# Optimization experiments

Hardware: AMD Instinct MI355X
Metric: run time of the kernel (lower is better)

Reference implementation:

```python
import jax, jax.numpy as jnp
import numpy as np

NUM_AUDIOS = 64
NODES_PER = 800
N = NUM_AUDIOS * NODES_PER  # 51200
DEG = 8
E = N * DEG  # 409600
IN_C, HID, OUT, HEADS = 512, 256, 256, 2
NEG_SLOPE = 0.2  # PyG GATConv default


def setup_inputs() -> dict:
    key = jax.random.key(0)
    ks = jax.random.split(key, 12)
    x = jax.random.normal(ks[0], (N, IN_C), jnp.float32)
    # edges strictly inside each audio's node block (PyG batching: no cross-graph edges)
    src_l = jax.random.randint(ks[1], (NUM_AUDIOS, NODES_PER * DEG), 0, NODES_PER)
    dst_l = jax.random.randint(ks[2], (NUM_AUDIOS, NODES_PER * DEG), 0, NODES_PER)
    off = (jnp.arange(NUM_AUDIOS) * NODES_PER)[:, None]
    edge_index = jnp.stack([(src_l + off).reshape(-1), (dst_l + off).reshape(-1)]).astype(jnp.int32)
    batch = jnp.repeat(jnp.arange(NUM_AUDIOS), NODES_PER).astype(jnp.int32)

    def gl(k, shape, fan):
        return (jax.random.normal(k, shape, jnp.float32) / np.sqrt(fan)).astype(jnp.float32)

    W1 = gl(ks[3], (IN_C, HEADS * HID), IN_C)
    a_s1 = gl(ks[4], (HEADS, HID), HID)
    a_d1 = gl(ks[5], (HEADS, HID), HID)
    b1 = jnp.zeros((HID,), jnp.float32)
    W2 = gl(ks[6], (HID, HEADS * OUT), HID)
    a_s2 = gl(ks[7], (HEADS, OUT), OUT)
    a_d2 = gl(ks[8], (HEADS, OUT), OUT)
    b2 = jnp.zeros((OUT,), jnp.float32)
    w_att = gl(ks[9], (OUT, 1), OUT)
    b_att = jnp.zeros((1,), jnp.float32)
    w_cls = gl(ks[10], (OUT, 2), OUT)
    b_cls = jnp.zeros((2,), jnp.float32)
    return dict(x=x, edge_index=edge_index, batch=batch,
                W1=W1, a_s1=a_s1, a_d1=a_d1, b1=b1,
                W2=W2, a_s2=a_s2, a_d2=a_d2, b2=b2,
                w_att=w_att, b_att=b_att, w_cls=w_cls, b_cls=b_cls)


def _gat(x, src, dst, W, a_s, a_d, b):
    """PyG GATConv(heads=H, concat=False): linear -> per-edge LeakyReLU scores ->
    softmax over incoming edges (with self-loops) -> scatter-sum -> head-mean + bias."""
    n = x.shape[0]
    H, C = a_s.shape
    h = (x @ W).reshape(n, H, C)                      # [N,H,C]
    al_s = jnp.einsum('nhc,hc->nh', h, a_s)           # [N,H]
    al_d = jnp.einsum('nhc,hc->nh', h, a_d)
    loop = jnp.arange(n, dtype=src.dtype)             # add self-loops (default)
    s = jnp.concatenate([src, loop])
    d = jnp.concatenate([dst, loop])
    e = jax.nn.leaky_relu(al_s[s] + al_d[d], NEG_SLOPE)  # [E+N,H]
    mx = jax.ops.segment_max(e, d, num_segments=n)
    w = jnp.exp(e - mx[d])
    den = jax.ops.segment_sum(w, d, num_segments=n)
    alpha = w / den[d]
    out = jax.ops.segment_sum(h[s] * alpha[:, :, None], d, num_segments=n)  # [N,H,C]
    return out.mean(axis=1) + b


def reference(x, edge_index, batch, W1, a_s1, a_d1, b1, W2, a_s2, a_d2, b2,
              w_att, b_att, w_cls, b_cls):
    src, dst = edge_index[0], edge_index[1]
    h = jax.nn.relu(_gat(x, src, dst, W1, a_s1, a_d1, b1))
    node_emb = _gat(h, src, dst, W2, a_s2, a_d2, b2)
    # per-audio temporal attention: softmax over nodes within each audio segment.
    # (edges never cross audio boundaries, so the per-subgraph GAT re-run in the
    #  original Python loop equals the full-graph GAT restricted to each segment.)
    logits = node_emb @ w_att + b_att                 # [N,1]
    mx = jax.ops.segment_max(logits, batch, num_segments=NUM_AUDIOS)
    w = jnp.exp(logits - mx[batch])
    den = jax.ops.segment_sum(w, batch, num_segments=NUM_AUDIOS)
    attn = w / den[batch]                             # [N,1]
    attended = jax.ops.segment_sum(attn * node_emb, batch, num_segments=NUM_AUDIOS)  # [A,OUT]
    audio_result = attended @ w_cls + b_cls           # [A,2]
    return node_emb, audio_result
```

## Files before the change

kernel.cpp:

```cpp
#include <hip/hip_runtime.h>
#include <cstdint>
#include <cstddef>

#define NUM_AUDIOS 64
#define NODES_PER  800
#define NN         51200
#define EE         409600

typedef __attribute__((ext_vector_type(8))) unsigned short ushort8;
typedef __attribute__((ext_vector_type(4))) unsigned short ushort4v;
typedef __attribute__((ext_vector_type(8))) __bf16 bf16x8;
typedef __attribute__((ext_vector_type(4))) float f32x4;

__device__ __forceinline__ float b2f(unsigned short h) {
  return __uint_as_float(((unsigned)h) << 16);
}
__device__ __forceinline__ unsigned short f2b(float f) {
  unsigned u = __float_as_uint(f);
  u += 0x7fffu + ((u >> 16) & 1u);
  return (unsigned short)(u >> 16);
}
__device__ __forceinline__ float lrelu(float v) { return v > 0.f ? v : 0.2f * v; }

#define P_AS1 0
#define P_AD1 512
#define P_B1  1024
#define P_AS2 1536
#define P_AD2 2048
#define P_B2  2560
#define P_WATT 3072
#define P_BATT 3328
#define P_WCLS 3336
#define P_BCLS 3848

#define ZERO_F4 132096
#define ZERO_BLOCKS 516

__global__ __launch_bounds__(256) void prolog0_k(float4* __restrict__ zbase,
                                                 const unsigned short* __restrict__ x,
                                                 int* __restrict__ flag) {
  const int i = blockIdx.x * 256 + threadIdx.x;
  if (i < ZERO_F4) zbase[i] = (float4){0.f, 0.f, 0.f, 0.f};
  if (blockIdx.x == 0) {
    __shared__ int s;
    if (threadIdx.x == 0) s = 0;
    __syncthreads();
    int big = 0;
    for (int k = threadIdx.x; k < 4096; k += 256) {
      const float v = b2f(x[k]);
      if (!(__builtin_fabsf(v) <= 1e4f)) big = 1;
    }
    if (big) atomicOr(&s, 1);
    __syncthreads();
    if (threadIdx.x == 0) *flag = s;
  }
}

#define PB_CONV 25600
#define PB_PAR  (PB_CONV + 10)
#define PB_T1   (PB_PAR + 1024)
#define PB_T2   (PB_T1 + 512)
#define PB_HIST (PB_T2 + 1600)

__global__ __launch_bounds__(256) void prep_k(
    const void* __restrict__ xraw, unsigned short* __restrict__ x16,
    const void* __restrict__ W1, unsigned short* __restrict__ W1T,
    const void* __restrict__ W2, unsigned short* __restrict__ W2T,
    const void* p0, const void* p1, const void* p2, const void* p3, const void* p4,
    const void* p5, const void* p6, const void* p7, const void* p8, const void* p9,
    unsigned short* __restrict__ params,
    const int* __restrict__ dst, int* __restrict__ counts,
    const int* __restrict__ flagp) {
  const int b = blockIdx.x, tid = threadIdx.x;
  const int f = *flagp;
  if (b < PB_CONV) {
    const size_t i = ((size_t)b * 256 + tid) * 4;
    if (f) {
      const float4 v = *(const float4*)((const float*)xraw + i);
      ushort4v o;
      o[0] = f2b(v.x); o[1] = f2b(v.y); o[2] = f2b(v.z); o[3] = f2b(v.w);
      *(ushort4v*)(x16 + i) = o;
    } else {
      *(ushort4v*)(x16 + i) = *(const ushort4v*)((const unsigned short*)xraw + i);
    }
  } else if (b < PB_PAR) {
    const void* srcs[10] = {p0, p1, p2, p3, p4, p5, p6, p7, p8, p9};
    const int offs[10] = {P_AS1, P_AD1, P_B1, P_AS2, P_AD2, P_B2, P_WATT, P_BATT, P_WCLS, P_BCLS};
    const int lens[10] = {512, 512, 256, 512, 512, 256, 256, 1, 512, 2};
    const int s = b - PB_CONV;
    for (int i = tid; i < lens[s]; i += 256)
      params[offs[s] + i] = f ? f2b(((const float*)srcs[s])[i])
                              : ((const unsigned short*)srcs[s])[i];
  } else if (b < PB_T1) {
    const int idx = (b - PB_PAR) * 256 + tid;
    const int n = idx >> 9, k = idx & 511;
    W1T[idx] = f ? f2b(((const float*)W1)[(size_t)k * 512 + n])
                 : ((const unsigned short*)W1)[(size_t)k * 512 + n];
  } else if (b < PB_T2) {
    const int idx = (b - PB_T1) * 256 + tid;
    const int n = idx >> 8, k = idx & 255;
    W2T[idx] = f ? f2b(((const float*)W2)[(size_t)k * 512 + n])
                 : ((const unsigned short*)W2)[(size_t)k * 512 + n];
  } else {
    const int e = (b - PB_T2) * 256 + tid;
    atomicAdd(&counts[dst[e]], 1);
  }
}

__global__ __launch_bounds__(256) void rowptr_k(const int* __restrict__ counts, int* __restrict__ row_ptr) {
  __shared__ int sh[800];
  __shared__ int pre[200];
  const int a = blockIdx.x, t = threadIdx.x;
  for (int i = t; i < 800; i += 256) sh[i] = counts[a * 800 + i];
  __syncthreads();
  if (t < 200) pre[t] = sh[t * 4] + sh[t * 4 + 1] + sh[t * 4 + 2] + sh[t * 4 + 3];
  __syncthreads();
  if (t == 0) {
    int run = 0;
    for (int i = 0; i < 200; ++i) { const int v = pre[i]; pre[i] = run; run += v; }
  }
  __syncthreads();
  if (t < 200) {
    int b = a * 6400 + pre[t];
#pragma unroll
    for (int j = 0; j < 4; ++j) { row_ptr[a * 800 + t * 4 + j] = b; b += sh[t * 4 + j]; }
  }
}

__global__ __launch_bounds__(256) void scatter_k(const int* __restrict__ src, const int* __restrict__ dst,
                                                 const int* __restrict__ row_ptr, int* __restrict__ cursor,
                                                 int* __restrict__ ssrc) {
  const int e = blockIdx.x * 256 + threadIdx.x;
  const int d = dst[e];
  const int p = atomicAdd(&cursor[d], 1);
  ssrc[row_ptr[d] + p] = src[e];
}

__global__ __launch_bounds__(256) void gemm_bt(const unsigned short* __restrict__ A,
                                               const unsigned short* __restrict__ BT,
                                               unsigned short* __restrict__ C,
                                               int K, int Nn,
                                               const unsigned short* __restrict__ a_s,
                                               const unsigned short* __restrict__ a_d,
                                               float* __restrict__ al_s,
                                               float* __restrict__ al_d) {
  __shared__ unsigned short As[128 * 32];
  __shared__ unsigned short Bs[128 * 32];
  const int tid = threadIdx.x;
  const int wave = tid >> 6, lane = tid & 63;
  const int m0 = blockIdx.y * 128, n0 = blockIdx.x * 128;
  const int wm = wave >> 1, wn = wave & 1;
  const int row = lane & 15, quad = lane >> 4;
  f32x4 acc[4][4];
#pragma unroll
  for (int i = 0; i < 4; ++i)
#pragma unroll
    for (int j = 0; j < 4; ++j) acc[i][j] = (f32x4){0.f, 0.f, 0.f, 0.f};

  for (int k0 = 0; k0 < K; k0 += 32) {
#pragma unroll
    for (int r = 0; r < 2; ++r) {
      const int cc = r * 256 + wave * 64 + lane;
      const int arow = cc >> 2, kc = (cc & 3) * 8;
      __builtin_amdgcn_global_load_lds(
          (const __attribute__((address_space(1))) void*)(A + (size_t)(m0 + arow) * K + k0 + kc),
          (__attribute__((address_space(3))) void*)(As + (size_t)(r * 256 + wave * 64) * 8),
          16, 0, 0);
      __builtin_amdgcn_global_load_lds(
          (const __attribute__((address_space(1))) void*)(BT + (size_t)(n0 + arow) * K + k0 + kc),
          (__attribute__((address_space(3))) void*)(Bs + (size_t)(r * 256 + wave * 64) * 8),
          16, 0, 0);
    }
    __syncthreads();

    bf16x8 af[4], bq[4];
#pragma unroll
    for (int i = 0; i < 4; ++i) {
      af[i] = *(const bf16x8*)&As[(wm * 64 + i * 16 + row) * 32 + quad * 8];
      bq[i] = *(const bf16x8*)&Bs[(wn * 64 + i * 16 + row) * 32 + quad * 8];
    }
#pragma unroll
    for (int i = 0; i < 4; ++i)
#pragma unroll
      for (int j = 0; j < 4; ++j)
        acc[i][j] = __builtin_amdgcn_mfma_f32_16x16x32_bf16(af[i], bq[j], acc[i][j], 0, 0, 0);
    __syncthreads();
  }

  const int col = lane & 15;
#pragma unroll
  for (int i = 0; i < 4; ++i)
#pragma unroll
    for (int j = 0; j < 4; ++j)
#pragma unroll
      for (int r = 0; r < 4; ++r) {
        const int gm = m0 + wm * 64 + i * 16 + quad * 4 + r;
        const int gn = n0 + wn * 64 + j * 16 + col;
        C[(size_t)gm * Nn + gn] = f2b(acc[i][j][r]);
      }

  {
    const int head = (n0 + wn * 64) >> 8;
    float as4[4], ad4[4];
#pragma unroll
    for (int j = 0; j < 4; ++j) {
      const int gn = n0 + wn * 64 + j * 16 + col;
      as4[j] = b2f(a_s[gn]);
      ad4[j] = b2f(a_d[gn]);
    }
#pragma unroll
    for (int i = 0; i < 4; ++i)
#pragma unroll
      for (int r = 0; r < 4; ++r) {
        float ps = 0.f, pd = 0.f;
#pragma unroll
        for (int j = 0; j < 4; ++j) { ps += acc[i][j][r] * as4[j]; pd += acc[i][j][r] * ad4[j]; }
#pragma unroll
        for (int off = 1; off < 16; off <<= 1) {
          ps += __shfl_xor(ps, off);
          pd += __shfl_xor(pd, off);
        }
        if (col == 0) {
          const int gm = m0 + wm * 64 + i * 16 + quad * 4 + r;
          atomicAdd(&al_s[gm * 2 + head], ps);
          atomicAdd(&al_d[gm * 2 + head], pd);
        }
      }
  }
}

__global__ __launch_bounds__(256) void agg_k(const unsigned short* __restrict__ h,
                                             const float* __restrict__ al_s, const float* __restrict__ al_d,
                                             const int* __restrict__ row_ptr, const int* __restrict__ counts,
                                             const int* __restrict__ ssrc, const unsigned short* __restrict__ bias,
                                             unsigned short* __restrict__ out, int do_relu,
                                             void* __restrict__ out2, const int* __restrict__ flagp,
                                             const unsigned short* __restrict__ watt,
                                             float* __restrict__ lg) {
  const int wave = threadIdx.x >> 6, lane = threadIdx.x & 63;
  const int b = blockIdx.x;
  const int g = b & 7, r = b >> 3;
  const int a = g + 8 * (r / 200);
  const int chunk = r % 200;
  const int n = a * 800 + chunk * 4 + wave;
  const int head = lane >> 5;
  const int hl = lane & 31;
  const int hsel = lane & 32;
  const int deg = counts[n];
  const int base = row_ptr[n];
  const float ald = al_d[n * 2 + head];
  const float self_e = lrelu(al_s[n * 2 + head] + ald);

  float m = -1e30f;
  for (int i = hl; i < deg; i += 32) {
    const int s = ssrc[base + i];
    m = fmaxf(m, al_s[s * 2 + head]);
  }
#pragma unroll
  for (int off = 1; off < 32; off <<= 1) m = fmaxf(m, __shfl_xor(m, off));
  const float mx = fmaxf(lrelu(m + ald), self_e);

  const float w_self = __expf(self_e - mx);
  float acc[8];
  {
    const ushort8 hv = *(const ushort8*)&h[(unsigned)(n * 512 + lane * 8)];
#pragma unroll
    for (int j = 0; j < 8; ++j) acc[j] = w_self * b2f(hv[j]);
  }
  float dpart = 0.f;
  for (int t0 = 0; t0 < deg; t0 += 32) {
    const int cnt = min(32, deg - t0);
    int s = 0; float w = 0.f;
    if (hl < cnt) {
      s = ssrc[base + t0 + hl];
      w = __expf(lrelu(al_s[s * 2 + head] + ald) - mx);
      dpart += w;
    }
    for (int i = 0; i < cnt; ++i) {
      const float wb = __shfl(w, hsel + i);
      const int sb = __shfl(s, hsel + i);
      const ushort8 hv = *(const ushort8*)&h[(unsigned)(sb * 512 + lane * 8)];
#pragma unroll
      for (int j = 0; j < 8; ++j) acc[j] += wb * b2f(hv[j]);
    }
  }
#pragma unroll
  for (int off = 1; off < 32; off <<= 1) dpart += __shfl_xor(dpart, off);
  const float inv = 1.f / (w_self + dpart);

  const int c0 = hl * 8;
  ushort8 res;
  float ov[8];
#pragma unroll
  for (int j = 0; j < 8; ++j) {
    const float mine = acc[j] * inv;
    const float other = __shfl_xor(mine, 32);
    float o = (mine + other) * 0.5f + b2f(bias[c0 + j]);
    if (do_relu) o = fmaxf(o, 0.f);
    ov[j] = o;
    res[j] = f2b(o);
  }
  if (lane < 32) {
    *(ushort8*)&out[(unsigned)(n * 256 + c0)] = res;
    if (out2) {
      if (*flagp) {
        float4* p = (float4*)((float*)out2 + (size_t)n * 256 + c0);
        p[0] = (float4){ov[0], ov[1], ov[2], ov[3]};
        p[1] = (float4){ov[4], ov[5], ov[6], ov[7]};
      } else {
        *(ushort8*)((unsigned short*)out2 + (size_t)n * 256 + c0) = res;
      }
    }
    if (lg) {
      const ushort8 wv = *(const ushort8*)&watt[c0];
      float d = 0.f;
#pragma unroll
      for (int j = 0; j < 8; ++j) d += ov[j] * b2f(wv[j]);
#pragma unroll
      for (int off = 1; off < 32; off <<= 1) d += __shfl_xor(d, off);
      if (hl == 0) lg[n] = d + b2f(watt[256]);
    }
  }
}

__global__ __launch_bounds__(256) void stats_k(const float* __restrict__ lg,
                                               float* __restrict__ mxv, float* __restrict__ invv) {
  __shared__ float red[256];
  const int a = blockIdx.x, t = threadIdx.x;
  float m = -1e30f;
  for (int i = t; i < 800; i += 256) m = fmaxf(m, lg[a * 800 + i]);
  red[t] = m; __syncthreads();
  for (int s = 128; s >= 1; s >>= 1) { if (t < s) red[t] = fmaxf(red[t], red[t + s]); __syncthreads(); }
  const float mx = red[0];
  __syncthreads();
  float sum = 0.f;
  for (int i = t; i < 800; i += 256) sum += __expf(lg[a * 800 + i] - mx);
  red[t] = sum; __syncthreads();
  for (int s = 128; s >= 1; s >>= 1) { if (t < s) red[t] += red[t + s]; __syncthreads(); }
  if (t == 0) { mxv[a] = mx; invv[a] = 1.f / red[0]; }
}

__global__ __launch_bounds__(256) void attended_k(const unsigned short* __restrict__ emb,
                                                  const float* __restrict__ lg,
                                                  const float* __restrict__ mxv,
                                                  const float* __restrict__ invv,
                                                  float* __restrict__ attended) {
  const int b = blockIdx.x;
  const int a = b >> 3, chunk = b & 7;
  const int t = threadIdx.x;
  __shared__ float ws[100];
  const int i0 = chunk * 100;
  const float mx = mxv[a], inv = invv[a];
  if (t < 100) ws[t] = __expf(lg[a * 800 + i0 + t] - mx) * inv;
  __syncthreads();
  float acc = 0.f;
  const unsigned short* base = emb + ((size_t)(a * 800 + i0)) * 256 + t;
#pragma unroll 4
  for (int j = 0; j < 100; ++j) acc += ws[j] * b2f(base[(size_t)j * 256]);
  atomicAdd(&attended[a * 256 + t], acc);
}

__global__ __launch_bounds__(256) void cls_k(const float* __restrict__ attended,
                                             const unsigned short* __restrict__ params,
                                             void* __restrict__ out, const int* __restrict__ flag) {
  __shared__ float red[256];
  const int a = blockIdx.x, t = threadIdx.x;
  const float v = attended[a * 256 + t];
  const float p0 = v * b2f(params[P_WCLS + t * 2]);
  const float p1 = v * b2f(params[P_WCLS + t * 2 + 1]);
  red[t] = p0; __syncthreads();
  for (int s = 128; s >= 1; s >>= 1) { if (t < s) red[t] += red[t + s]; __syncthreads(); }
  const float r0 = red[0];
  __syncthreads();
  red[t] = p1; __syncthreads();
  for (int s = 128; s >= 1; s >>= 1) { if (t < s) red[t] += red[t + s]; __syncthreads(); }
  const float r1 = red[0];
  if (t == 0) {
    const float o0 = r0 + b2f(params[P_BCLS]);
    const float o1 = r1 + b2f(params[P_BCLS + 1]);
    if (*flag) {
      ((float*)out)[(size_t)NN * 256 + a * 2]     = o0;
      ((float*)out)[(size_t)NN * 256 + a * 2 + 1] = o1;
    } else {
      ((unsigned short*)out)[(size_t)NN * 256 + a * 2]     = f2b(o0);
      ((unsigned short*)out)[(size_t)NN * 256 + a * 2 + 1] = f2b(o1);
    }
  }
}

extern "C" void kernel_launch(void* const* d_in, const int* in_sizes, int n_in,
                              void* d_out, int out_size, void* d_ws, size_t ws_size,
                              hipStream_t stream) {
  (void)in_sizes; (void)n_in; (void)out_size; (void)ws_size;
  const void* x_raw  = d_in[0];
  const int*  eidx   = (const int*)d_in[1];
  const int* src = eidx;
  const int* dst = eidx + EE;

  char* ws = (char*)d_ws;
  size_t off = 0;
  auto alloc = [&](size_t bytes) -> void* {
    void* p = ws + off;
    off += (bytes + 255) & ~(size_t)255;
    return p;
  };
  int* flag              = (int*)alloc(256);
  unsigned short* params = (unsigned short*)alloc(4096 * 2);
  unsigned short* W1T    = (unsigned short*)alloc((size_t)512 * 512 * 2);
  unsigned short* W2T    = (unsigned short*)alloc((size_t)512 * 256 * 2);
  unsigned short* x16    = (unsigned short*)alloc((size_t)NN * 512 * 2);
  unsigned short* hbig   = (unsigned short*)alloc((size_t)NN * 512 * 2);
  int*   counts   = (int*)alloc((size_t)NN * 4);
  int*   cursor   = (int*)alloc((size_t)NN * 4);
  float* attended = (float*)alloc((size_t)NUM_AUDIOS * 256 * 4);
  float* al_s1    = (float*)alloc((size_t)NN * 2 * 4);
  float* al_d1    = (float*)alloc((size_t)NN * 2 * 4);
  float* al_s2    = (float*)alloc((size_t)NN * 2 * 4);
  float* al_d2    = (float*)alloc((size_t)NN * 2 * 4);
  int*   rowp   = (int*)alloc((size_t)NN * 4);
  int*   ssrc   = (int*)alloc((size_t)EE * 4);
  float* lg     = (float*)alloc((size_t)NN * 4);
  float* mxv    = (float*)alloc(NUM_AUDIOS * 4);
  float* invv   = (float*)alloc(NUM_AUDIOS * 4);
  unsigned short* hrel  = x16;
  unsigned short* emb16 = x16 + (size_t)NN * 256;

  prolog0_k<<<dim3(ZERO_BLOCKS), 256, 0, stream>>>((float4*)counts,
                                                   (const unsigned short*)x_raw, flag);

  prep_k<<<dim3(PB_HIST), 256, 0, stream>>>(
      x_raw, x16, d_in[3], W1T, d_in[7], W2T,
      d_in[4], d_in[5], d_in[6], d_in[8], d_in[9],
      d_in[10], d_in[11], d_in[12], d_in[13], d_in[14],
      params, dst, counts, flag);

  rowptr_k<<<dim3(NUM_AUDIOS), 256, 0, stream>>>(counts, rowp);
  scatter_k<<<dim3(EE / 256), 256, 0, stream>>>(src, dst, rowp, cursor, ssrc);

  gemm_bt<<<dim3(4, 400), 256, 0, stream>>>(x16, W1T, hbig, 512, 512,
                                            params + P_AS1, params + P_AD1, al_s1, al_d1);
  agg_k<<<dim3(NN / 4), 256, 0, stream>>>(hbig, al_s1, al_d1, rowp, counts, ssrc,
                                          params + P_B1, hrel, 1, nullptr, flag,
                                          params + P_WATT, nullptr);

  gemm_bt<<<dim3(4, 400), 256, 0, stream>>>(hrel, W2T, hbig, 256, 512,
                                            params + P_AS2, params + P_AD2, al_s2, al_d2);
  agg_k<<<dim3(NN / 4), 256, 0, stream>>>(hbig, al_s2, al_d2, rowp, counts, ssrc,
                                          params + P_B2, emb16, 0, d_out, flag,
                                          params + P_WATT, lg);

  stats_k<<<dim3(NUM_AUDIOS), 256, 0, stream>>>(lg, mxv, invv);
  attended_k<<<dim3(NUM_AUDIOS * 8), 256, 0, stream>>>(emb16, lg, mxv, invv, attended);
  cls_k<<<dim3(NUM_AUDIOS), 256, 0, stream>>>(attended, params, d_out, flag);
}
```

Before: 440.4 us.

## Fuse fp32-to-bf16 input conversion into GEMM loads, swizzle LDS, remap block order

```diff
diff --git a/kernel.cpp b/kernel.cpp
--- a/kernel.cpp
+++ b/kernel.cpp
@@ -56,14 +56,12 @@
   }
 }
 
-#define PB_CONV 25600
-#define PB_PAR  (PB_CONV + 10)
+#define PB_PAR  10
 #define PB_T1   (PB_PAR + 1024)
 #define PB_T2   (PB_T1 + 512)
 #define PB_HIST (PB_T2 + 1600)
 
 __global__ __launch_bounds__(256) void prep_k(
-    const void* __restrict__ xraw, unsigned short* __restrict__ x16,
     const void* __restrict__ W1, unsigned short* __restrict__ W1T,
     const void* __restrict__ W2, unsigned short* __restrict__ W2T,
     const void* p0, const void* p1, const void* p2, const void* p3, const void* p4,
@@ -73,21 +71,11 @@
     const int* __restrict__ flagp) {
   const int b = blockIdx.x, tid = threadIdx.x;
   const int f = *flagp;
-  if (b < PB_CONV) {
-    const size_t i = ((size_t)b * 256 + tid) * 4;
-    if (f) {
-      const float4 v = *(const float4*)((const float*)xraw + i);
-      ushort4v o;
-      o[0] = f2b(v.x); o[1] = f2b(v.y); o[2] = f2b(v.z); o[3] = f2b(v.w);
-      *(ushort4v*)(x16 + i) = o;
-    } else {
-      *(ushort4v*)(x16 + i) = *(const ushort4v*)((const unsigned short*)xraw + i);
-    }
-  } else if (b < PB_PAR) {
+  if (b < PB_PAR) {
     const void* srcs[10] = {p0, p1, p2, p3, p4, p5, p6, p7, p8, p9};
     const int offs[10] = {P_AS1, P_AD1, P_B1, P_AS2, P_AD2, P_B2, P_WATT, P_BATT, P_WCLS, P_BCLS};
     const int lens[10] = {512, 512, 256, 512, 512, 256, 256, 1, 512, 2};
-    const int s = b - PB_CONV;
+    const int s = b;
     for (int i = tid; i < lens[s]; i += 256)
       params[offs[s] + i] = f ? f2b(((const float*)srcs[s])[i])
                               : ((const unsigned short*)srcs[s])[i];
@@ -136,19 +124,39 @@
   ssrc[row_ptr[d] + p] = src[e];
 }
 
-__global__ __launch_bounds__(256) void gemm_bt(const unsigned short* __restrict__ A,
+__device__ __forceinline__ void mfma_tile(const unsigned short* As, const unsigned short* Bs,
+                                          int wm, int wn, int row, int quad, f32x4 acc[4][4]) {
+  bf16x8 af[4], bq[4];
+  const int pa = (quad ^ (row & 3)) * 8;
+#pragma unroll
+  for (int i = 0; i < 4; ++i) {
+    af[i] = *(const bf16x8*)&As[(wm * 64 + i * 16 + row) * 32 + pa];
+    bq[i] = *(const bf16x8*)&Bs[(wn * 64 + i * 16 + row) * 32 + pa];
+  }
+#pragma unroll
+  for (int i = 0; i < 4; ++i)
+#pragma unroll
+    for (int j = 0; j < 4; ++j)
+      acc[i][j] = __builtin_amdgcn_mfma_f32_16x16x32_bf16(af[i], bq[j], acc[i][j], 0, 0, 0);
+}
+
+__global__ __launch_bounds__(256) void gemm_bt(const void* __restrict__ Araw,
                                                const unsigned short* __restrict__ BT,
                                                unsigned short* __restrict__ C,
                                                int K, int Nn,
                                                const unsigned short* __restrict__ a_s,
                                                const unsigned short* __restrict__ a_d,
                                                float* __restrict__ al_s,
-                                               float* __restrict__ al_d) {
+                                               float* __restrict__ al_d,
+                                               const int* __restrict__ aflag) {
   __shared__ unsigned short As[128 * 32];
   __shared__ unsigned short Bs[128 * 32];
   const int tid = threadIdx.x;
   const int wave = tid >> 6, lane = tid & 63;
-  const int m0 = blockIdx.y * 128, n0 = blockIdx.x * 128;
+  const int bid = blockIdx.x;
+  const int g = bid & 7, bt = bid >> 3;
+  const int m0 = (g * 50 + (bt >> 2)) * 128;
+  const int n0 = (bt & 3) * 128;
   const int wm = wave >> 1, wn = wave & 1;
   const int row = lane & 15, quad = lane >> 4;
   f32x4 acc[4][4];
@@ -157,34 +165,58 @@
 #pragma unroll
     for (int j = 0; j < 4; ++j) acc[i][j] = (f32x4){0.f, 0.f, 0.f, 0.f};
 
-  for (int k0 = 0; k0 < K; k0 += 32) {
-#pragma unroll
-    for (int r = 0; r < 2; ++r) {
-      const int cc = r * 256 + wave * 64 + lane;
-      const int arow = cc >> 2, kc = (cc & 3) * 8;
-      __builtin_amdgcn_global_load_lds(
-          (const __attribute__((address_space(1))) void*)(A + (size_t)(m0 + arow) * K + k0 + kc),
-          (__attribute__((address_space(3))) void*)(As + (size_t)(r * 256 + wave * 64) * 8),
-          16, 0, 0);
-      __builtin_amdgcn_global_load_lds(
-          (const __attribute__((address_space(1))) void*)(BT + (size_t)(n0 + arow) * K + k0 + kc),
-          (__attribute__((address_space(3))) void*)(Bs + (size_t)(r * 256 + wave * 64) * 8),
-          16, 0, 0);
-    }
-    __syncthreads();
-
-    bf16x8 af[4], bq[4];
-#pragma unroll
-    for (int i = 0; i < 4; ++i) {
-      af[i] = *(const bf16x8*)&As[(wm * 64 + i * 16 + row) * 32 + quad * 8];
-      bq[i] = *(const bf16x8*)&Bs[(wn * 64 + i * 16 + row) * 32 + quad * 8];
-    }
-#pragma unroll
-    for (int i = 0; i < 4; ++i)
-#pragma unroll
-      for (int j = 0; j < 4; ++j)
-        acc[i][j] = __builtin_amdgcn_mfma_f32_16x16x32_bf16(af[i], bq[j], acc[i][j], 0, 0, 0);
-    __syncthreads();
+  const bool a_is_f32 = (aflag != nullptr) && (*aflag != 0);
+  const unsigned short* A16 = (const unsigned short*)Araw;
+  const float* A32 = (const float*)Araw;
+  const int srow0 = tid >> 2;
+  const int kph = tid & 3;
+
+  if (!a_is_f32) {
+    for (int k0 = 0; k0 < K; k0 += 32) {
+      __syncthreads();
+#pragma unroll
+      for (int r = 0; r < 2; ++r) {
+        const int arow = r * 64 + srow0;
+        const int kc = ((kph ^ (arow & 3)) * 8);
+        __builtin_amdgcn_global_load_lds(
+            (const __attribute__((address_space(1))) void*)(A16 + (size_t)(m0 + arow) * K + k0 + kc),
+            (__attribute__((address_space(3))) void*)(As + (size_t)(r * 256 + wave * 64) * 8),
+            16, 0, 0);
+        __builtin_amdgcn_global_load_lds(
+            (const __attribute__((address_space(1))) void*)(BT + (size_t)(n0 + arow) * K + k0 + kc),
+            (__attribute__((address_space(3))) void*)(Bs + (size_t)(r * 256 + wave * 64) * 8),
+            16, 0, 0);
+      }
+      __syncthreads();
+      mfma_tile(As, Bs, wm, wn, row, quad, acc);
+    }
+  } else {
+    for (int k0 = 0; k0 < K; k0 += 32) {
+      ushort8 pk[2];
+#pragma unroll
+      for (int r = 0; r < 2; ++r) {
+        const int arow = r * 64 + srow0;
+        const int kc = ((kph ^ (arow & 3)) * 8);
+        const float* p = A32 + (size_t)(m0 + arow) * K + k0 + kc;
+        const float4 f0 = *(const float4*)p;
+        const float4 f1 = *(const float4*)(p + 4);
+        pk[r][0] = f2b(f0.x); pk[r][1] = f2b(f0.y); pk[r][2] = f2b(f0.z); pk[r][3] = f2b(f0.w);
+        pk[r][4] = f2b(f1.x); pk[r][5] = f2b(f1.y); pk[r][6] = f2b(f1.z); pk[r][7] = f2b(f1.w);
+      }
+      __syncthreads();
+#pragma unroll
+      for (int r = 0; r < 2; ++r) {
+        const int arow = r * 64 + srow0;
+        const int kc = ((kph ^ (arow & 3)) * 8);
+        __builtin_amdgcn_global_load_lds(
+            (const __attribute__((address_space(1))) void*)(BT + (size_t)(n0 + arow) * K + k0 + kc),
+            (__attribute__((address_space(3))) void*)(Bs + (size_t)(r * 256 + wave * 64) * 8),
+            16, 0, 0);
+        *(ushort8*)&As[(size_t)(r * 256 + tid) * 8] = pk[r];
+      }
+      __syncthreads();
+      mfma_tile(As, Bs, wm, wn, row, quad, acc);
+    }
   }
 
   const int col = lane & 15;
@@ -408,7 +440,7 @@
   unsigned short* params = (unsigned short*)alloc(4096 * 2);
   unsigned short* W1T    = (unsigned short*)alloc((size_t)512 * 512 * 2);
   unsigned short* W2T    = (unsigned short*)alloc((size_t)512 * 256 * 2);
-  unsigned short* x16    = (unsigned short*)alloc((size_t)NN * 512 * 2);
+  unsigned short* scr    = (unsigned short*)alloc((size_t)NN * 512 * 2);
   unsigned short* hbig   = (unsigned short*)alloc((size_t)NN * 512 * 2);
   int*   counts   = (int*)alloc((size_t)NN * 4);
   int*   cursor   = (int*)alloc((size_t)NN * 4);
@@ -422,14 +454,14 @@
   float* lg     = (float*)alloc((size_t)NN * 4);
   float* mxv    = (float*)alloc(NUM_AUDIOS * 4);
   float* invv   = (float*)alloc(NUM_AUDIOS * 4);
-  unsigned short* hrel  = x16;
-  unsigned short* emb16 = x16 + (size_t)NN * 256;
+  unsigned short* hrel  = scr;
+  unsigned short* emb16 = scr + (size_t)NN * 256;
 
   prolog0_k<<<dim3(ZERO_BLOCKS), 256, 0, stream>>>((float4*)counts,
                                                    (const unsigned short*)x_raw, flag);
 
   prep_k<<<dim3(PB_HIST), 256, 0, stream>>>(
-      x_raw, x16, d_in[3], W1T, d_in[7], W2T,
+      d_in[3], W1T, d_in[7], W2T,
       d_in[4], d_in[5], d_in[6], d_in[8], d_in[9],
       d_in[10], d_in[11], d_in[12], d_in[13], d_in[14],
       params, dst, counts, flag);
@@ -437,14 +469,14 @@
   rowptr_k<<<dim3(NUM_AUDIOS), 256, 0, stream>>>(counts, rowp);
   scatter_k<<<dim3(EE / 256), 256, 0, stream>>>(src, dst, rowp, cursor, ssrc);
 
-  gemm_bt<<<dim3(4, 400), 256, 0, stream>>>(x16, W1T, hbig, 512, 512,
-                                            params + P_AS1, params + P_AD1, al_s1, al_d1);
+  gemm_bt<<<dim3(1600), 256, 0, stream>>>(x_raw, W1T, hbig, 512, 512,
+                                          params + P_AS1, params + P_AD1, al_s1, al_d1, flag);
   agg_k<<<dim3(NN / 4), 256, 0, stream>>>(hbig, al_s1, al_d1, rowp, counts, ssrc,
                                           params + P_B1, hrel, 1, nullptr, flag,
                                           params + P_WATT, nullptr);
 
-  gemm_bt<<<dim3(4, 400), 256, 0, stream>>>(hrel, W2T, hbig, 256, 512,
-                                            params + P_AS2, params + P_AD2, al_s2, al_d2);
+  gemm_bt<<<dim3(1600), 256, 0, stream>>>(hrel, W2T, hbig, 256, 512,
+                                          params + P_AS2, params + P_AD2, al_s2, al_d2, nullptr);
   agg_k<<<dim3(NN / 4), 256, 0, stream>>>(hbig, al_s2, al_d2, rowp, counts, ssrc,
                                           params + P_B2, emb16, 0, d_out, flag,
                                           params + P_WATT, lg);
```

After: 438.9 us. Within noise of the previous version (-0.3%).
